# Kernel tuning notes

Measured on AMD Instinct MI355X. Metric: run time of the kernel, lower is better.

## Reference

```python
import jax, jax.numpy as jnp
import numpy as np

B, N, C = 2, 2048, 1024
H = 16
D = C // H  # head_dim = 64
SCALE = D ** -0.5


def setup_inputs() -> dict:
    key = jax.random.key(0)
    ks = jax.random.split(key, 9)
    s = C ** -0.5  # ~ torch Linear default init scale
    return {
        "x": jax.random.normal(ks[0], (B, N, C), dtype=jnp.float32),
        "Wq": jax.random.uniform(ks[1], (C, C), jnp.float32, -s, s),
        "bq": jax.random.uniform(ks[2], (C,), jnp.float32, -s, s),
        "Wk": jax.random.uniform(ks[3], (C, C), jnp.float32, -s, s),
        "bk": jax.random.uniform(ks[4], (C,), jnp.float32, -s, s),
        "Wv": jax.random.uniform(ks[5], (C, C), jnp.float32, -s, s),
        "bv": jax.random.uniform(ks[6], (C,), jnp.float32, -s, s),
        "Wo": jax.random.uniform(ks[7], (C, C), jnp.float32, -s, s),
        "bo": jax.random.uniform(ks[8], (C,), jnp.float32, -s, s),
    }


def reference(x, Wq, bq, Wk, bk, Wv, bv, Wo, bo):
    # Projections: [B,N,C] -> [B,H,N,D]
    def split_heads(t):
        return t.reshape(B, N, H, D).transpose(0, 2, 1, 3)

    q = split_heads(x @ Wq.T + bq)
    k = split_heads(x @ Wk.T + bk)
    v = split_heads(x @ Wv.T + bv)

    scores = jnp.einsum("bhnd,bhmd->bhnm", q, k) * SCALE  # [B,H,N,N]
    attn = jax.nn.softmax(scores, axis=-1)
    out = jnp.einsum("bhnm,bhmd->bhnd", attn, v)  # [B,H,N,D]
    out = out.transpose(0, 2, 1, 3).reshape(B, N, C)
    return out @ Wo.T + bo
```

## Files before the change

kernel.cpp:

```cpp
#include <hip/hip_runtime.h>
#include <stdint.h>


typedef _Float16 h8 __attribute__((ext_vector_type(8)));
typedef _Float16 h4 __attribute__((ext_vector_type(4)));
typedef float f4 __attribute__((ext_vector_type(4)));
typedef float f16f __attribute__((ext_vector_type(16)));
typedef uint32_t u32;
typedef u32 u32x4 __attribute__((ext_vector_type(4)));

#define AS1(p) ((const __attribute__((address_space(1))) void*)(p))
#define AS3(p) ((__attribute__((address_space(3))) void*)(p))

template <int ITERS>
__device__ __forceinline__ void stage128B(const _Float16* g, int ldk, _Float16* s, int tid) {
#pragma unroll
  for (int j = 0; j < ITERS; ++j) {
    int off = j * 4096 + tid * 16;
    int row = off >> 7;
    int ch = (off >> 4) & 7;
    int gch = ch ^ (row & 7);
    __builtin_amdgcn_global_load_lds(AS1(g + row * ldk + gch * 8), AS3(s + (off >> 1)), 16, 0, 0);
  }
}

__device__ __forceinline__ void stage_v(const _Float16* g, _Float16* s, int tid) {
#pragma unroll
  for (int j = 0; j < 2; ++j) {
    int off = j * 4096 + tid * 16;
    int row = off >> 7;
    int ch = (off >> 4) & 7;
    int gch = ch ^ (row & 7);
    __builtin_amdgcn_global_load_lds(AS1(g + row * 2048 + gch * 8), AS3(s + (off >> 1)), 16, 0, 0);
  }
}
__device__ __forceinline__ void stage_k(const _Float16* g, _Float16* s, int tid) {
#pragma unroll
  for (int j = 0; j < 2; ++j) {
    int off = j * 4096 + tid * 16;
    int row = off >> 7;
    int ch = (off >> 4) & 7;
    int gch = ch ^ ((row & 3) | ((row >> 1) & 4));
    __builtin_amdgcn_global_load_lds(AS1(g + row * 64 + gch * 8), AS3(s + (off >> 1)), 16, 0, 0);
  }
}

__device__ __forceinline__ h8 frag64(const _Float16* s, int row, int g) {
  return *(const h8*)(s + row * 64 + ((g ^ (row & 7)) << 3));
}

__global__ void cvt_all(const float* __restrict__ x, const float* __restrict__ Wq,
                        const float* __restrict__ Wk, const float* __restrict__ Wv,
                        const float* __restrict__ Wo, _Float16* __restrict__ xh,
                        _Float16* __restrict__ q, _Float16* __restrict__ k,
                        _Float16* __restrict__ v, _Float16* __restrict__ o) {
  int blk = blockIdx.x;
  const float* src; _Float16* dst; int off;
  if (blk < 2048)      { src = x;  dst = xh; off = blk; }
  else if (blk < 2560) { src = Wq; dst = q;  off = blk - 2048; }
  else if (blk < 3072) { src = Wk; dst = k;  off = blk - 2560; }
  else if (blk < 3584) { src = Wv; dst = v;  off = blk - 3072; }
  else                 { src = Wo; dst = o;  off = blk - 3584; }
  int i = off * 2048 + threadIdx.x * 8;
  f4 a = *(const f4*)(src + i);
  f4 b = *(const f4*)(src + i + 4);
  h8 ov;
  ov[0] = (_Float16)a[0]; ov[1] = (_Float16)a[1]; ov[2] = (_Float16)a[2]; ov[3] = (_Float16)a[3];
  ov[4] = (_Float16)b[0]; ov[5] = (_Float16)b[1]; ov[6] = (_Float16)b[2]; ov[7] = (_Float16)b[3];
  *(h8*)(dst + i) = ov;
}

__global__ __launch_bounds__(256, 3) void gemm_qkv(
    const _Float16* __restrict__ X,
    const _Float16* __restrict__ W0, const _Float16* __restrict__ W1, const _Float16* __restrict__ W2,
    const float* __restrict__ b0, const float* __restrict__ b1, const float* __restrict__ b2,
    _Float16* __restrict__ O0, _Float16* __restrict__ O1, _Float16* __restrict__ O2) {
  __shared__ _Float16 As[128 * 64];
  __shared__ _Float16 Bs[128 * 64];
  int z = blockIdx.z;
  const _Float16* W = (z == 0) ? W0 : (z == 1) ? W1 : W2;
  const float* bias = (z == 0) ? b0 : (z == 1) ? b1 : b2;

  int tid = threadIdx.x;
  int lane = tid & 63, wave = tid >> 6;
  int quad = lane >> 4, l15 = lane & 15;
  int wm = (wave >> 1) << 6, wn = (wave & 1) << 6;
  int m0 = blockIdx.y << 7, n0 = blockIdx.x << 7;

  f4 acc[4][4] = {};
  for (int k0 = 0; k0 < 1024; k0 += 64) {
    stage128B<4>(X + m0 * 1024 + k0, 1024, As, tid);
    stage128B<4>(W + n0 * 1024 + k0, 1024, Bs, tid);
    __syncthreads();
#pragma unroll
    for (int ks = 0; ks < 2; ++ks) {
      h8 af[4], bf[4];
#pragma unroll
      for (int i = 0; i < 4; ++i) af[i] = frag64(As, wm + i * 16 + l15, ks * 4 + quad);
#pragma unroll
      for (int i = 0; i < 4; ++i) bf[i] = frag64(Bs, wn + i * 16 + l15, ks * 4 + quad);
#pragma unroll
      for (int mi = 0; mi < 4; ++mi)
#pragma unroll
        for (int ni = 0; ni < 4; ++ni)
          acc[mi][ni] = __builtin_amdgcn_mfma_f32_16x16x32_f16(af[mi], bf[ni], acc[mi][ni], 0, 0, 0);
    }
    __syncthreads();
  }

  if (z == 2) {
#pragma unroll
    for (int mi = 0; mi < 4; ++mi) {
#pragma unroll
      for (int ni = 0; ni < 4; ++ni) {
        int o = n0 + wn + ni * 16 + l15;
        float bv = bias[o];
        int h = o >> 6, dd = o & 63;
        int m = m0 + wm + mi * 16 + quad * 4;
        int b = m >> 11, n = m & 2047;
        h4 v;
#pragma unroll
        for (int r = 0; r < 4; ++r) v[r] = (_Float16)(acc[mi][ni][r] + bv);
        *(h4*)(O2 + (((b * 16 + h) * 64 + dd) * 2048 + n)) = v;
      }
    }
  } else {
    float scale = (z == 0) ? 0.125f * 1.44269504089f : 1.0f;
    _Float16* Out = (z == 0) ? O0 : O1;
#pragma unroll
    for (int mi = 0; mi < 4; ++mi) {
#pragma unroll
      for (int ni = 0; ni < 4; ++ni) {
        int o = n0 + wn + ni * 16 + l15;
        float bv = bias[o];
        int h = o >> 6, d = o & 63;
#pragma unroll
        for (int r = 0; r < 4; ++r) {
          int m = m0 + wm + mi * 16 + quad * 4 + r;
          int b = m >> 11, n = m & 2047;
          float v = (acc[mi][ni][r] + bv) * scale;
          Out[(((b * 16 + h) * 2048 + n) << 6) + d] = (_Float16)v;
        }
      }
    }
  }
}

__global__ __launch_bounds__(256, 3) void gemm_out(
    const _Float16* __restrict__ A, const _Float16* __restrict__ W,
    const float* __restrict__ bias, float* __restrict__ Out) {
  __shared__ _Float16 As[128 * 64];
  __shared__ _Float16 Bs[64 * 64];
  int tid = threadIdx.x;
  int lane = tid & 63, wave = tid >> 6;
  int quad = lane >> 4, l15 = lane & 15;
  int wm = (wave >> 1) << 6, wn = (wave & 1) << 5;
  int m0 = blockIdx.y << 7, n0 = blockIdx.x << 6;

  f4 acc[4][2] = {};
  for (int k0 = 0; k0 < 1024; k0 += 64) {
    stage128B<4>(A + m0 * 1024 + k0, 1024, As, tid);
    stage128B<2>(W + n0 * 1024 + k0, 1024, Bs, tid);
    __syncthreads();
#pragma unroll
    for (int ks = 0; ks < 2; ++ks) {
      h8 af[4], bf[2];
#pragma unroll
      for (int i = 0; i < 4; ++i) af[i] = frag64(As, wm + i * 16 + l15, ks * 4 + quad);
#pragma unroll
      for (int i = 0; i < 2; ++i) bf[i] = frag64(Bs, wn + i * 16 + l15, ks * 4 + quad);
#pragma unroll
      for (int mi = 0; mi < 4; ++mi)
#pragma unroll
        for (int ni = 0; ni < 2; ++ni)
          acc[mi][ni] = __builtin_amdgcn_mfma_f32_16x16x32_f16(af[mi], bf[ni], acc[mi][ni], 0, 0, 0);
    }
    __syncthreads();
  }
#pragma unroll
  for (int mi = 0; mi < 4; ++mi) {
#pragma unroll
    for (int ni = 0; ni < 2; ++ni) {
      int o = n0 + wn + ni * 16 + l15;
      float bv = bias[o];
#pragma unroll
      for (int r = 0; r < 4; ++r) {
        int m = m0 + wm + mi * 16 + quad * 4 + r;
        Out[m * 1024 + o] = acc[mi][ni][r] + bv;
      }
    }
  }
}

__global__ __launch_bounds__(256, 2) void attn(
    const _Float16* __restrict__ Q, const _Float16* __restrict__ Kv,
    const _Float16* __restrict__ Vt, _Float16* __restrict__ AO) {
  __shared__ _Float16 smem[6 * 4096];
  _Float16* Ksb = smem;
  _Float16* Vsb = smem + 3 * 4096;

  int tid = threadIdx.x, lane = tid & 63, wave = tid >> 6;
  int h = lane >> 5, l31 = lane & 31;
  int p = wave & 1, qg = wave >> 1;

  int flat = blockIdx.y * 16 + blockIdx.x;
  int nid = (flat & 7) * 64 + (flat >> 3);
  int bh = nid >> 4, q0 = (nid & 15) << 7;

  const _Float16* Qb = Q + (bh * 2048 + q0 + qg * 64 + l31) * 64;
  h8 qf[2][4];
#pragma unroll
  for (int qs = 0; qs < 2; ++qs)
#pragma unroll
    for (int ks4 = 0; ks4 < 4; ++ks4)
      qf[qs][ks4] = *(const h8*)(Qb + qs * 32 * 64 + ks4 * 16 + h * 8);

  int krow = (l31 & 19) | ((l31 & 4) << 1) | ((l31 & 8) >> 1);
  int kbase = (p * 32 + krow) * 64;
  int kx = (krow & 3) | ((krow >> 1) & 4);
  int vx = l31 & 7;

  const _Float16* Kb = Kv + bh * 131072;
  const _Float16* Vb = Vt + bh * 131072;
  f16f oacc[2][2] = {};
  float lsum[2] = {0.f, 0.f};

  stage_k(Kb, Ksb, tid);
  stage_v(Vb, Vsb, tid);
  stage_k(Kb + 4096, Ksb + 4096, tid);
  stage_v(Vb + 64, Vsb + 4096, tid);

  int bp = 0;
  for (int ph = 0; ph < 32; ++ph) {
    if (ph < 31) {
      asm volatile("s_waitcnt vmcnt(4)\n\ts_barrier" ::: "memory");
    } else {
      asm volatile("s_waitcnt vmcnt(0)\n\ts_barrier" ::: "memory");
    }
    const _Float16* Kst = Ksb + bp * 4096;
    const _Float16* Vst = Vsb + bp * 4096;

    f16f sacc[2] = {};
#pragma unroll
    for (int ks4 = 0; ks4 < 4; ++ks4) {
      h8 kf = *(const h8*)(Kst + kbase + (((ks4 * 2 + h) ^ kx) << 3));
      sacc[0] = __builtin_amdgcn_mfma_f32_32x32x16_f16(kf, qf[0][ks4], sacc[0], 0, 0, 0);
      sacc[1] = __builtin_amdgcn_mfma_f32_32x32x16_f16(kf, qf[1][ks4], sacc[1], 0, 0, 0);
    }

    u32 pkw[2][8];
#pragma unroll
    for (int qs = 0; qs < 2; ++qs) {
#pragma unroll
      for (int i = 0; i < 8; ++i) {
        float pa = __builtin_amdgcn_exp2f(sacc[qs][2 * i]);
        float pb = __builtin_amdgcn_exp2f(sacc[qs][2 * i + 1]);
        lsum[qs] += pa + pb;
        pkw[qs][i] = __builtin_bit_cast(u32, __builtin_amdgcn_cvt_pkrtz(pa, pb));
      }
    }

#pragma unroll
    for (int s = 0; s < 2; ++s) {
      u32x4 pw0 = {pkw[0][4 * s], pkw[0][4 * s + 1], pkw[0][4 * s + 2], pkw[0][4 * s + 3]};
      u32x4 pw1 = {pkw[1][4 * s], pkw[1][4 * s + 1], pkw[1][4 * s + 2], pkw[1][4 * s + 3]};
      h8 pb0 = __builtin_bit_cast(h8, pw0);
      h8 pb1 = __builtin_bit_cast(h8, pw1);
      int ch = (((p << 2) | (s << 1) | h) ^ vx) << 3;
#pragma unroll
      for (int dt = 0; dt < 2; ++dt) {
        h8 vf = *(const h8*)(Vst + (dt * 32 + l31) * 64 + ch);
        oacc[0][dt] = __builtin_amdgcn_mfma_f32_32x32x16_f16(vf, pb0, oacc[0][dt], 0, 0, 0);
        oacc[1][dt] = __builtin_amdgcn_mfma_f32_32x32x16_f16(vf, pb1, oacc[1][dt], 0, 0, 0);
      }
    }

    if (ph < 30) {
      int sl = bp ? bp - 1 : 2;
      stage_k(Kb + (ph + 2) * 4096, Ksb + sl * 4096, tid);
      stage_v(Vb + (ph + 2) * 64, Vsb + sl * 4096, tid);
    }
    bp = (bp == 2) ? 0 : bp + 1;
  }

  __syncthreads();
  float* cb = (float*)smem;
  if (p) {
    float* w = cb + (qg * 64 + lane) * 66;
#pragma unroll
    for (int qs = 0; qs < 2; ++qs)
#pragma unroll
      for (int dt = 0; dt < 2; ++dt)
#pragma unroll
        for (int i = 0; i < 16; ++i) w[(qs * 2 + dt) * 16 + i] = oacc[qs][dt][i];
    w[64] = lsum[0];
    w[65] = lsum[1];
  }
  __syncthreads();
  if (!p) {
    const float* r = cb + (qg * 64 + lane) * 66;
#pragma unroll
    for (int qs = 0; qs < 2; ++qs)
#pragma unroll
      for (int dt = 0; dt < 2; ++dt)
#pragma unroll
        for (int i = 0; i < 16; ++i) oacc[qs][dt][i] += r[(qs * 2 + dt) * 16 + i];
    lsum[0] += r[64];
    lsum[1] += r[65];

    int b = bh >> 4, hh = bh & 15;
#pragma unroll
    for (int qs = 0; qs < 2; ++qs) {
      float l = lsum[qs] + __shfl_xor(lsum[qs], 32);
      float inv = 1.0f / l;
      int n = q0 + qg * 64 + qs * 32 + l31;
      _Float16* base = AO + (b * 2048 + n) * 1024 + hh * 64;
#pragma unroll
      for (int dt = 0; dt < 2; ++dt) {
#pragma unroll
        for (int b2 = 0; b2 < 4; ++b2) {
          h4 o;
#pragma unroll
          for (int a = 0; a < 4; ++a) o[a] = (_Float16)(oacc[qs][dt][b2 * 4 + a] * inv);
          *(h4*)(base + dt * 32 + b2 * 8 + h * 4) = o;
        }
      }
    }
  }
}

extern "C" void kernel_launch(void* const* d_in, const int* in_sizes, int n_in,
                              void* d_out, int out_size, void* d_ws, size_t ws_size,
                              hipStream_t stream) {
  const float* x = (const float*)d_in[0];
  const float* Wq = (const float*)d_in[1];
  const float* bq = (const float*)d_in[2];
  const float* Wk = (const float*)d_in[3];
  const float* bk = (const float*)d_in[4];
  const float* Wv = (const float*)d_in[5];
  const float* bv = (const float*)d_in[6];
  const float* Wo = (const float*)d_in[7];
  const float* bo = (const float*)d_in[8];
  float* out = (float*)d_out;

  char* w = (char*)d_ws;
  _Float16* xh  = (_Float16*)(w);
  _Float16* Wqh = (_Float16*)(w + (8u << 20));
  _Float16* Wkh = (_Float16*)(w + (10u << 20));
  _Float16* Wvh = (_Float16*)(w + (12u << 20));
  _Float16* Woh = (_Float16*)(w + (14u << 20));
  _Float16* Qh  = (_Float16*)(w + (16u << 20));
  _Float16* Kh  = (_Float16*)(w + (24u << 20));
  _Float16* Vth = (_Float16*)(w + (32u << 20));
  _Float16* AOh = xh;

  cvt_all<<<4096, 256, 0, stream>>>(x, Wq, Wk, Wv, Wo, xh, Wqh, Wkh, Wvh, Woh);
  gemm_qkv<<<dim3(8, 32, 3), 256, 0, stream>>>(xh, Wqh, Wkh, Wvh, bq, bk, bv, Qh, Kh, Vth);
  attn<<<dim3(16, 32), 256, 0, stream>>>(Qh, Kh, Vth, AOh);
  gemm_out<<<dim3(16, 32), 256, 0, stream>>>(AOh, Woh, bo, out);
}
```

Baseline: 175.4 us.

## Remap GEMM block order for XCD locality and vectorize Q/K epilogue stores

Both projection GEMMs now remap the flat block index so that consecutive blocks landing on the same XCD (round-robin by 8) get adjacent tiles, aiming to improve L2 reuse of shared A/W panels. For Q and K outputs, the MFMA operands are swapped to produce a transposed accumulator. Each lane then holds 4 consecutive head-dim values and can emit h4 vector stores with a vectorized bias load, replacing scalar scattered half stores. This adds index arithmetic and a branch on z inside the inner loop, which could affect code size and register pressure.

```diff
diff --git a/kernel.cpp b/kernel.cpp
--- a/kernel.cpp
+++ b/kernel.cpp
@@ -77,7 +77,13 @@
     _Float16* __restrict__ O0, _Float16* __restrict__ O1, _Float16* __restrict__ O2) {
   __shared__ _Float16 As[128 * 64];
   __shared__ _Float16 Bs[128 * 64];
-  int z = blockIdx.z;
+
+  int flat = blockIdx.x + 8 * (blockIdx.y + 32 * blockIdx.z);
+  int nid = (flat & 7) * 96 + (flat >> 3);
+  int z = nid >> 8;
+  int rem = nid & 255;
+  int by = rem >> 3, bx = rem & 7;
+
   const _Float16* W = (z == 0) ? W0 : (z == 1) ? W1 : W2;
   const float* bias = (z == 0) ? b0 : (z == 1) ? b1 : b2;
 
@@ -85,7 +91,7 @@
   int lane = tid & 63, wave = tid >> 6;
   int quad = lane >> 4, l15 = lane & 15;
   int wm = (wave >> 1) << 6, wn = (wave & 1) << 6;
-  int m0 = blockIdx.y << 7, n0 = blockIdx.x << 7;
+  int m0 = by << 7, n0 = bx << 7;
 
   f4 acc[4][4] = {};
   for (int k0 = 0; k0 < 1024; k0 += 64) {
@@ -99,11 +105,19 @@
       for (int i = 0; i < 4; ++i) af[i] = frag64(As, wm + i * 16 + l15, ks * 4 + quad);
 #pragma unroll
       for (int i = 0; i < 4; ++i) bf[i] = frag64(Bs, wn + i * 16 + l15, ks * 4 + quad);
-#pragma unroll
-      for (int mi = 0; mi < 4; ++mi)
-#pragma unroll
-        for (int ni = 0; ni < 4; ++ni)
-          acc[mi][ni] = __builtin_amdgcn_mfma_f32_16x16x32_f16(af[mi], bf[ni], acc[mi][ni], 0, 0, 0);
+      if (z == 2) {
+#pragma unroll
+        for (int mi = 0; mi < 4; ++mi)
+#pragma unroll
+          for (int ni = 0; ni < 4; ++ni)
+            acc[mi][ni] = __builtin_amdgcn_mfma_f32_16x16x32_f16(af[mi], bf[ni], acc[mi][ni], 0, 0, 0);
+      } else {
+#pragma unroll
+        for (int mi = 0; mi < 4; ++mi)
+#pragma unroll
+          for (int ni = 0; ni < 4; ++ni)
+            acc[ni][mi] = __builtin_amdgcn_mfma_f32_16x16x32_f16(bf[ni], af[mi], acc[ni][mi], 0, 0, 0);
+      }
     }
     __syncthreads();
   }
@@ -128,19 +142,18 @@
     float scale = (z == 0) ? 0.125f * 1.44269504089f : 1.0f;
     _Float16* Out = (z == 0) ? O0 : O1;
 #pragma unroll
-    for (int mi = 0; mi < 4; ++mi) {
-#pragma unroll
-      for (int ni = 0; ni < 4; ++ni) {
-        int o = n0 + wn + ni * 16 + l15;
-        float bv = bias[o];
-        int h = o >> 6, d = o & 63;
-#pragma unroll
-        for (int r = 0; r < 4; ++r) {
-          int m = m0 + wm + mi * 16 + quad * 4 + r;
-          int b = m >> 11, n = m & 2047;
-          float v = (acc[mi][ni][r] + bv) * scale;
-          Out[(((b * 16 + h) * 2048 + n) << 6) + d] = (_Float16)v;
-        }
+    for (int ni = 0; ni < 4; ++ni) {
+      int o0 = n0 + wn + ni * 16 + quad * 4;
+      f4 bv4 = *(const f4*)(bias + o0);
+      int hh = o0 >> 6, d = o0 & 63;
+#pragma unroll
+      for (int mi = 0; mi < 4; ++mi) {
+        int m = m0 + wm + mi * 16 + l15;
+        int b = m >> 11, n = m & 2047;
+        h4 v;
+#pragma unroll
+        for (int r = 0; r < 4; ++r) v[r] = (_Float16)((acc[ni][mi][r] + bv4[r]) * scale);
+        *(h4*)(Out + (((b * 16 + hh) * 2048 + n) << 6) + d) = v;
       }
     }
   }
@@ -155,7 +168,11 @@
   int lane = tid & 63, wave = tid >> 6;
   int quad = lane >> 4, l15 = lane & 15;
   int wm = (wave >> 1) << 6, wn = (wave & 1) << 5;
-  int m0 = blockIdx.y << 7, n0 = blockIdx.x << 6;
+
+  int flat = blockIdx.x + (blockIdx.y << 4);
+  int nid = (flat & 7) * 64 + (flat >> 3);
+  int n0 = (nid & 15) << 6;
+  int m0 = (nid >> 4) << 7;
 
   f4 acc[4][2] = {};
   for (int k0 = 0; k0 < 1024; k0 += 64) {
```

New measurement: 218.9 us. +24.8%, slower.
